# Kernel tuning notes

Hardware: AMD Instinct MI355X
Metric: run time of the kernel (lower is better)

## Reference

```python
import jax, jax.numpy as jnp
import numpy as np

C = 256      # bev_channels
K = 5        # deform kernel size
PAD = K // 2
T = K * K    # 25 taps
MID = C // 8 # channel-attn bottleneck
H, W = 100, 100
B = 1
GN_GROUPS = 8
EPS = 1e-5


def conv1x1(x, w, b=None):
    # x [B,Ci,H,W], w [Co,Ci]
    y = jnp.einsum('oc,bchw->bohw', w, x)
    if b is not None:
        y = y + b[None, :, None, None]
    return y


def conv3x3(x, w):
    # x [B,Ci,H,W], w [Co,Ci,3,3], stride 1, SAME padding
    return jax.lax.conv_general_dilated(
        x, w, (1, 1), 'SAME', dimension_numbers=('NCHW', 'OIHW', 'NCHW'))


def group_norm(x, gamma, beta, groups=GN_GROUPS, eps=EPS):
    b, c, h, w = x.shape
    xg = x.reshape(b, groups, c // groups, h, w)
    m = xg.mean((2, 3, 4), keepdims=True)
    v = xg.var((2, 3, 4), keepdims=True)
    xg = (xg - m) * jax.lax.rsqrt(v + eps)
    return xg.reshape(b, c, h, w) * gamma[None, :, None, None] + beta[None, :, None, None]


def deform_dw_conv(hist, offset, weight):
    """Depthwise deformable conv (torchvision semantics, deform_groups=1).
    hist [B,C,H,W], offset [B,2*T,H,W] as (dy,dx) pairs per tap (row-major taps),
    weight [C,1,K,K]. Zero-padding outside image (bilinear corners masked)."""
    b, c, h, w = hist.shape
    off = offset.reshape(b, T, 2, h, w)
    hg, wg = jnp.meshgrid(jnp.arange(h, dtype=hist.dtype),
                          jnp.arange(w, dtype=hist.dtype), indexing='ij')
    ky = (jnp.arange(T) // K - PAD).astype(hist.dtype)
    kx = (jnp.arange(T) % K - PAD).astype(hist.dtype)
    ys = hg[None, None] + ky[None, :, None, None] + off[:, :, 0]  # [B,T,H,W]
    xs = wg[None, None] + kx[None, :, None, None] + off[:, :, 1]

    def sample(img, yy, xx):  # img [C,H,W]; yy,xx [T,H,W]
        y0 = jnp.floor(yy)
        x0 = jnp.floor(xx)

        def gather(yc, xc):
            valid = (yc >= 0) & (yc <= h - 1) & (xc >= 0) & (xc <= w - 1)
            yi = jnp.clip(yc, 0, h - 1).astype(jnp.int32)
            xi = jnp.clip(xc, 0, w - 1).astype(jnp.int32)
            v = img.reshape(c, -1)[:, (yi * w + xi).reshape(-1)].reshape(c, T, h, w)
            return jnp.where(valid[None], v, jnp.zeros((), img.dtype))

        wy = yy - y0
        wx = xx - x0
        return (((1 - wy) * (1 - wx))[None] * gather(y0, x0)
                + ((1 - wy) * wx)[None] * gather(y0, x0 + 1)
                + (wy * (1 - wx))[None] * gather(y0 + 1, x0)
                + (wy * wx)[None] * gather(y0 + 1, x0 + 1))

    sampled = jax.vmap(sample)(hist, ys, xs)  # [B,C,T,H,W]
    return jnp.einsum('bcthw,ct->bchw', sampled, weight.reshape(c, T))


def ha_net(cur, hist, offset_w, offset_b, deform_w, ca_w1, ca_w2, out_w, gn_g, gn_b):
    offset = conv1x1(jnp.concatenate([cur, hist], axis=1), offset_w, offset_b)
    aligned = deform_dw_conv(hist, offset, deform_w)
    pooled = (cur - aligned).mean((2, 3))                    # AdaptiveAvgPool2d(1) -> [B,C]
    attn = jax.nn.sigmoid(jax.nn.relu(pooled @ ca_w1.T) @ ca_w2.T)[:, :, None, None]
    fused = cur + aligned * attn
    return jax.nn.relu(group_norm(conv3x3(fused, out_w), gn_g, gn_b))


def setup_inputs() -> dict:
    key = jax.random.key(0)
    ks = jax.random.split(key, 12)
    rn = lambda k, s, sc: jax.random.normal(k, s, jnp.float32) * sc
    return {
        'cur':   rn(ks[0], (B, C, H, W), 1.0),
        'hist0': rn(ks[1], (B, C, H, W), 1.0),
        'hist1': rn(ks[2], (B, C, H, W), 1.0),
        'offset_w': rn(ks[3], (2 * T, 2 * C), 0.01),
        'offset_b': jnp.zeros((2 * T,), jnp.float32),
        'deform_w': rn(ks[4], (C, 1, K, K), 0.2),
        'ca_w1': rn(ks[5], (MID, C), 0.05),
        'ca_w2': rn(ks[6], (C, MID), 0.05),
        'out_w': rn(ks[7], (C, C, 3, 3), 0.02),
        'gn_g': jnp.ones((C,), jnp.float32),
        'gn_b': jnp.zeros((C,), jnp.float32),
        'fuse_w': rn(ks[8], (C, C, 3, 3), 0.02),
        'bn_g': jnp.ones((C,), jnp.float32),
        'bn_b': jnp.zeros((C,), jnp.float32),
    }


def reference(cur, hist0, hist1, offset_w, offset_b, deform_w, ca_w1, ca_w2,
              out_w, gn_g, gn_b, fuse_w, bn_g, bn_b):
    aligned_sum = 0.0
    weight_sum = 0.0
    for hist in (hist0, hist1):  # fixed memory length = 2
        aligned = ha_net(cur, hist, offset_w, offset_b, deform_w,
                         ca_w1, ca_w2, out_w, gn_g, gn_b)
        diff = jnp.abs(cur - hist).mean((2, 3), keepdims=True)  # [B,C,1,1]
        wgt = jax.nn.sigmoid(-diff)
        aligned_sum = aligned_sum + aligned * wgt
        weight_sum = weight_sum + wgt
    fused = aligned_sum / (weight_sum + 1e-6)
    # fuse_conv: Conv3x3 -> BatchNorm2d (training: batch stats) -> ReLU
    y = conv3x3(fused, fuse_w)
    m = y.mean((0, 2, 3))
    v = y.var((0, 2, 3))
    y = (y - m[None, :, None, None]) * jax.lax.rsqrt(v + EPS)[None, :, None, None]
    y = y * bn_g[None, :, None, None] + bn_b[None, :, None, None]
    return jax.nn.relu(y)
```

## Files before the change

kernel.cpp:

```cpp
#include <hip/hip_runtime.h>
#include <hip/hip_bf16.h>

#define HW 10000
#define NC 256

typedef _Float16 h8 __attribute__((ext_vector_type(8)));
typedef float f32x4 __attribute__((ext_vector_type(4)));

#define RS 40

__device__ __forceinline__ int swz(int pos, int chunk) {
  return pos * RS + ((chunk ^ (pos & 3)) << 3);
}

#define WS_WMF     0
#define WS_ALIGNED 294912
#define WS_YBUF    2854912
#define WS_ASUM    5414912
#define WS_WOF     7974912
#define WS_POOLED  8007680
#define WS_ATTN    8007936
#define WS_WGT     8008192
#define WS_INVW    8008704
#define WS_GMV     8008960
#define WS_GNP     8008976

__device__ __forceinline__ float block_sum(float v, volatile float* sh) {
#pragma unroll
  for (int o = 32; o > 0; o >>= 1) v += __shfl_down(v, o);
  __syncthreads();
  if ((threadIdx.x & 63) == 0) sh[threadIdx.x >> 6] = v;
  __syncthreads();
  return sh[0] + sh[1] + sh[2] + sh[3];
}

__global__ void wprep_half(const float* __restrict__ W, int half, h8* __restrict__ Wmf) {
  const int id = blockIdx.x * 256 + threadIdx.x;
  const int lane = id & 63;
  int rest = id >> 6;
  const int s = rest & 1; rest >>= 1;
  const int tap = rest % 9; rest /= 9;
  const int c = rest & 7;
  const int cogl = rest >> 3;
  const int co = (half * 8 + cogl) * 16 + (lane & 15);
  const int ci0 = c * 32 + (lane >> 4) * 8;
  h8 frag;
#pragma unroll
  for (int j = 0; j < 8; j++) {
    const float w = W[(co * 256 + ci0 + j) * 9 + tap];
    const _Float16 hi = (_Float16)w;
    frag[j] = (s == 0) ? hi : (_Float16)((w - (float)hi) * 2048.f);
  }
  Wmf[id] = frag;
}

__global__ void wprep2(const float* __restrict__ W, h8* __restrict__ Wof) {
  const int id = blockIdx.x * 256 + threadIdx.x;
  const int lane = id & 63;
  int rest = id >> 6;
  const int g = rest & 3; rest >>= 2;
  const int s = rest & 1;
  const int c = rest >> 1;
  const int co = g * 16 + (lane & 15);
  const int ci0 = c * 32 + (lane >> 4) * 8;
  h8 frag;
#pragma unroll
  for (int j = 0; j < 8; j++) {
    const float w = (co < 50) ? W[co * 512 + ci0 + j] : 0.f;
    const _Float16 hi = (_Float16)w;
    frag[j] = (s == 0) ? hi : (_Float16)((w - (float)hi) * 2048.f);
  }
  Wof[id] = frag;
}

__global__ void gemm1x1_mfma(const float* __restrict__ cur, const float* __restrict__ hist,
                             const h8* __restrict__ Wof, const float* __restrict__ bias,
                             float* __restrict__ out) {
  __shared__ alignas(16) _Float16 Phi[64 * RS];
  __shared__ alignas(16) _Float16 Plo[64 * RS];
  const int t = threadIdx.x, lane = t & 63, wave = t >> 6;
  const int p0 = blockIdx.x * 64;
  const int nl = lane & 15, ksub = lane >> 4;
  f32x4 accM[4], accC[4], accL[4];
#pragma unroll
  for (int g = 0; g < 4; g++) { accM[g] = (f32x4)0.f; accC[g] = (f32x4)0.f; accL[g] = (f32x4)0.f; }
  const int bbase = swz(16 * wave + nl, ksub);

  for (int c = 0; c < 16; c++) {
    __syncthreads();
    for (int idx = t; idx < 1024; idx += 256) {
      const int cp = idx >> 6;
      const int pos = idx & 63;
      const int ci = c * 32 + cp * 2;
      const int p = p0 + pos;
      float v0 = 0.f, v1 = 0.f;
      if (p < HW) {
        v0 = (ci < NC) ? cur[ci * HW + p] : hist[(ci - NC) * HW + p];
        v1 = (ci + 1 < NC) ? cur[(ci + 1) * HW + p] : hist[(ci + 1 - NC) * HW + p];
      }
      const _Float16 h0 = (_Float16)v0, h1 = (_Float16)v1;
      const _Float16 l0 = (_Float16)((v0 - (float)h0) * 2048.f);
      const _Float16 l1 = (_Float16)((v1 - (float)h1) * 2048.f);
      const unsigned uh = (unsigned)__builtin_bit_cast(unsigned short, h0) |
                          ((unsigned)__builtin_bit_cast(unsigned short, h1) << 16);
      const unsigned ul = (unsigned)__builtin_bit_cast(unsigned short, l0) |
                          ((unsigned)__builtin_bit_cast(unsigned short, l1) << 16);
      const int ea = swz(pos, cp >> 2) + ((cp & 3) << 1);
      *(unsigned*)&Phi[ea] = uh;
      *(unsigned*)&Plo[ea] = ul;
    }
    __syncthreads();
    const h8 Bh = *(const h8*)&Phi[bbase];
    const h8 Bl = *(const h8*)&Plo[bbase];
#pragma unroll
    for (int g = 0; g < 4; g++) {
      const h8 Ah = Wof[((c * 2 + 0) * 4 + g) * 64 + lane];
      const h8 Al = Wof[((c * 2 + 1) * 4 + g) * 64 + lane];
      accM[g] = __builtin_amdgcn_mfma_f32_16x16x32_f16(Ah, Bh, accM[g], 0, 0, 0);
      accC[g] = __builtin_amdgcn_mfma_f32_16x16x32_f16(Ah, Bl, accC[g], 0, 0, 0);
      accC[g] = __builtin_amdgcn_mfma_f32_16x16x32_f16(Al, Bh, accC[g], 0, 0, 0);
      accL[g] = __builtin_amdgcn_mfma_f32_16x16x32_f16(Al, Bl, accL[g], 0, 0, 0);
    }
  }
#pragma unroll
  for (int g = 0; g < 4; g++) {
#pragma unroll
    for (int j = 0; j < 4; j++) {
      const int co = g * 16 + ksub * 4 + j;
      const int p = p0 + 16 * wave + nl;
      if (co < 50 && p < HW)
        out[co * HW + p] = accM[g][j] + accC[g][j] * (1.f / 2048.f) +
                           accL[g][j] * (1.f / 4194304.f) + bias[co];
    }
  }
}

__global__ void deform_kernel(const float* __restrict__ hist, const float* __restrict__ off,
                              const float* __restrict__ dw, float* __restrict__ aligned) {
  const int lane = threadIdx.x & 63;
  const int sub = threadIdx.x >> 6;
  const int p = blockIdx.x * 64 + lane;
  if (p >= HW) return;
  const int y = p / 100;
  const int x = p - y * 100;
  const int cbase = blockIdx.y * 32 + sub * 8;
  float acc[8];
#pragma unroll
  for (int k = 0; k < 8; k++) acc[k] = 0.f;

  for (int t = 0; t < 25; t++) {
    const float dy = off[(2 * t) * HW + p];
    const float dx = off[(2 * t + 1) * HW + p];
    const float ys = (float)(y + t / 5 - 2) + dy;
    const float xs = (float)(x + t % 5 - 2) + dx;
    const float y0f = floorf(ys), x0f = floorf(xs);
    const int y0 = (int)y0f, x0 = (int)x0f;
    const float wy = ys - y0f, wx = xs - x0f;
    const bool vy0 = (y0 >= 0) && (y0 <= 99);
    const bool vy1 = (y0 + 1 >= 0) && (y0 + 1 <= 99);
    const bool vx0 = (x0 >= 0) && (x0 <= 99);
    const bool vx1 = (x0 + 1 >= 0) && (x0 + 1 <= 99);
    const float w00 = (vy0 && vx0) ? (1.f - wy) * (1.f - wx) : 0.f;
    const float w01 = (vy0 && vx1) ? (1.f - wy) * wx : 0.f;
    const float w10 = (vy1 && vx0) ? wy * (1.f - wx) : 0.f;
    const float w11 = (vy1 && vx1) ? wy * wx : 0.f;
    const int yc0 = min(max(y0, 0), 99), yc1 = min(max(y0 + 1, 0), 99);
    const int xc0 = min(max(x0, 0), 99), xc1 = min(max(x0 + 1, 0), 99);
    const int i00 = yc0 * 100 + xc0, i01 = yc0 * 100 + xc1;
    const int i10 = yc1 * 100 + xc0, i11 = yc1 * 100 + xc1;
#pragma unroll
    for (int k = 0; k < 8; k++) {
      const float* hp = hist + (cbase + k) * HW;
      const float s = w00 * hp[i00] + w01 * hp[i01] + w10 * hp[i10] + w11 * hp[i11];
      acc[k] += dw[(cbase + k) * 25 + t] * s;
    }
  }
#pragma unroll
  for (int k = 0; k < 8; k++) aligned[(cbase + k) * HW + p] = acc[k];
}

__global__ void reduce_pw(const float* __restrict__ cur, const float* __restrict__ aligned,
                          const float* __restrict__ hist, float* __restrict__ pooled,
                          float* __restrict__ wgt) {
  __shared__ float sh[4];
  const int c = blockIdx.x;
  float s1 = 0.f, s2 = 0.f;
  for (int i = threadIdx.x; i < HW; i += 256) {
    const float cv = cur[c * HW + i];
    s1 += cv - aligned[c * HW + i];
    s2 += fabsf(cv - hist[c * HW + i]);
  }
  s1 = block_sum(s1, sh);
  s2 = block_sum(s2, sh);
  if (threadIdx.x == 0) {
    pooled[c] = s1 * (1.f / (float)HW);
    wgt[c] = 1.f / (1.f + expf(s2 * (1.f / (float)HW)));
  }
}

__global__ void attn_kernel(const float* __restrict__ pooled, const float* __restrict__ w1,
                            const float* __restrict__ w2, float* __restrict__ attn) {
  __shared__ float pl[256], hid[32];
  const int t = threadIdx.x;
  pl[t] = pooled[t];
  __syncthreads();
  if (t < 32) {
    float s = 0.f;
    for (int c = 0; c < 256; c++) s += w1[t * 256 + c] * pl[c];
    hid[t] = fmaxf(s, 0.f);
  }
  __syncthreads();
  float s = 0.f;
#pragma unroll
  for (int m = 0; m < 32; m++) s += w2[t * 32 + m] * hid[m];
  attn[t] = 1.f / (1.f + expf(-s));
}

__global__ void conv3x3_mfma(const float* __restrict__ X, const float* __restrict__ sx,
                             const float* __restrict__ Y, const h8* __restrict__ Wmf,
                             int half, float* __restrict__ out) {
  __shared__ alignas(16) _Float16 Phi[100 * RS];
  __shared__ alignas(16) _Float16 Plo[100 * RS];
  const int t = threadIdx.x, lane = t & 63, wave = t >> 6;
  const int ox0 = blockIdx.x * 8, oy0 = blockIdx.y * 8;
  const int wc = wave & 1, wn = wave >> 1;
  const int px0 = lane & 7, pyr = (lane >> 3) & 1, ksub = lane >> 4;

  f32x4 accM[4][2], accC[4][2], accL[4][2];
#pragma unroll
  for (int g = 0; g < 4; g++)
#pragma unroll
    for (int n = 0; n < 2; n++) {
      accM[g][n] = (f32x4)0.f; accC[g][n] = (f32x4)0.f; accL[g][n] = (f32x4)0.f;
    }

  int pbase[2];
#pragma unroll
  for (int n = 0; n < 2; n++)
    pbase[n] = (2 * (2 * wn + n) + pyr) * 10 + px0;

  for (int c = 0; c < 8; c++) {
    __syncthreads();
    for (int idx = t; idx < 1600; idx += 256) {
      const int cp = idx / 100;
      const int pos = idx - cp * 100;
      const int py = pos / 10, px = pos - py * 10;
      const int gy = oy0 - 1 + py, gx = ox0 - 1 + px;
      const int ci = c * 32 + cp * 2;
      float v0 = 0.f, v1 = 0.f;
      if (gy >= 0 && gy < 100 && gx >= 0 && gx < 100) {
        const int gi = gy * 100 + gx;
        v0 = X[ci * HW + gi] * sx[ci];
        v1 = X[(ci + 1) * HW + gi] * sx[ci + 1];
        if (Y) { v0 += Y[ci * HW + gi]; v1 += Y[(ci + 1) * HW + gi]; }
      }
      const _Float16 h0 = (_Float16)v0, h1 = (_Float16)v1;
      const _Float16 l0 = (_Float16)((v0 - (float)h0) * 2048.f);
      const _Float16 l1 = (_Float16)((v1 - (float)h1) * 2048.f);
      const unsigned uh = (unsigned)__builtin_bit_cast(unsigned short, h0) |
                          ((unsigned)__builtin_bit_cast(unsigned short, h1) << 16);
      const unsigned ul = (unsigned)__builtin_bit_cast(unsigned short, l0) |
                          ((unsigned)__builtin_bit_cast(unsigned short, l1) << 16);
      const int ea = swz(pos, cp >> 2) + ((cp & 3) << 1);
      *(unsigned*)&Phi[ea] = uh;
      *(unsigned*)&Plo[ea] = ul;
    }
    __syncthreads();
#pragma unroll
    for (int ky = 0; ky < 3; ky++) {
#pragma unroll
      for (int kx = 0; kx < 3; kx++) {
        const int tap = ky * 3 + kx;
        h8 Bh[2], Bl[2];
#pragma unroll
        for (int n = 0; n < 2; n++) {
          const int ba = swz(pbase[n] + ky * 10 + kx, ksub);
          Bh[n] = *(const h8*)&Phi[ba];
          Bl[n] = *(const h8*)&Plo[ba];
        }
#pragma unroll
        for (int g = 0; g < 4; g++) {
          const int cogl = wc * 4 + g;
          const h8* wp = Wmf + (size_t)(((cogl * 8 + c) * 9 + tap) * 2) * 64 + lane;
          const h8 Ah = wp[0];
          const h8 Al = wp[64];
#pragma unroll
          for (int n = 0; n < 2; n++) {
            accM[g][n] = __builtin_amdgcn_mfma_f32_16x16x32_f16(Ah, Bh[n], accM[g][n], 0, 0, 0);
            accC[g][n] = __builtin_amdgcn_mfma_f32_16x16x32_f16(Ah, Bl[n], accC[g][n], 0, 0, 0);
            accC[g][n] = __builtin_amdgcn_mfma_f32_16x16x32_f16(Al, Bh[n], accC[g][n], 0, 0, 0);
            accL[g][n] = __builtin_amdgcn_mfma_f32_16x16x32_f16(Al, Bl[n], accL[g][n], 0, 0, 0);
          }
        }
      }
    }
  }
#pragma unroll
  for (int g = 0; g < 4; g++) {
#pragma unroll
    for (int n = 0; n < 2; n++) {
      const int oy = oy0 + 2 * (2 * wn + n) + pyr;
      const int ox = ox0 + px0;
#pragma unroll
      for (int j = 0; j < 4; j++) {
        const int co = (half * 8 + wc * 4 + g) * 16 + ksub * 4 + j;
        if (oy < 100 && ox < 100)
          out[co * HW + oy * 100 + ox] = accM[g][n][j] + accC[g][n][j] * (1.f / 2048.f) +
                                         accL[g][n][j] * (1.f / 4194304.f);
      }
    }
  }
}

__global__ void gn_partial(const float* __restrict__ y, float* __restrict__ part) {
  __shared__ float sh[4];
  const int bx = blockIdx.x;
  const float* base = y + (size_t)bx * 4 * HW;
  float s = 0.f, ss = 0.f;
  for (int i = threadIdx.x; i < 4 * HW; i += 256) {
    const float v = base[i];
    s += v; ss += v * v;
  }
  s = block_sum(s, sh);
  ss = block_sum(ss, sh);
  if (threadIdx.x == 0) { part[bx] = s; part[64 + bx] = ss; }
}

__global__ void gn_final(const float* __restrict__ part, float* __restrict__ gmv) {
  const int g = threadIdx.x;
  if (g < 8) {
    float s = 0.f, ss = 0.f;
#pragma unroll
    for (int j = 0; j < 8; j++) { s += part[g * 8 + j]; ss += part[64 + g * 8 + j]; }
    const float m = s * (1.f / 320000.f);
    const float var = ss * (1.f / 320000.f) - m * m;
    gmv[g] = m;
    gmv[8 + g] = rsqrtf(var + 1e-5f);
  }
}

__global__ void gn_apply(const float* __restrict__ y, const float* __restrict__ gmv,
                         const float* __restrict__ gn_g, const float* __restrict__ gn_b,
                         const float* __restrict__ wgt, float* __restrict__ asum, int first) {
  const int c = blockIdx.x;
  const int g = c >> 5;
  const float m = gmv[g], rs = gmv[8 + g], ga = gn_g[c], be = gn_b[c], wg = wgt[c];
  for (int i = threadIdx.x; i < HW; i += 256) {
    const float v = fmaxf((y[c * HW + i] - m) * rs * ga + be, 0.f) * wg;
    if (first) asum[c * HW + i] = v;
    else asum[c * HW + i] += v;
  }
}

__global__ void invw_kernel(const float* __restrict__ wgt, float* __restrict__ invw) {
  const int c = threadIdx.x;
  invw[c] = 1.f / (wgt[c] + wgt[256 + c] + 1e-6f);
}

__global__ void bn_relu(const float* __restrict__ y, const float* __restrict__ bn_g,
                        const float* __restrict__ bn_b, float* __restrict__ out) {
  __shared__ float sh[4];
  const int c = blockIdx.x;
  float s = 0.f;
  for (int i = threadIdx.x; i < HW; i += 256) s += y[c * HW + i];
  const float m = block_sum(s, sh) * (1.f / (float)HW);
  float ss = 0.f;
  for (int i = threadIdx.x; i < HW; i += 256) {
    const float d = y[c * HW + i] - m;
    ss += d * d;
  }
  const float var = block_sum(ss, sh) * (1.f / (float)HW);
  const float rstd = rsqrtf(var + 1e-5f);
  const float ga = bn_g[c], be = bn_b[c];
  for (int i = threadIdx.x; i < HW; i += 256) {
    out[c * HW + i] = fmaxf((y[c * HW + i] - m) * rstd * ga + be, 0.f);
  }
}

extern "C" void kernel_launch(void* const* d_in, const int* in_sizes, int n_in,
                              void* d_out, int out_size, void* d_ws, size_t ws_size,
                              hipStream_t stream) {
  const float* cur      = (const float*)d_in[0];
  const float* hist0    = (const float*)d_in[1];
  const float* hist1    = (const float*)d_in[2];
  const float* offset_w = (const float*)d_in[3];
  const float* offset_b = (const float*)d_in[4];
  const float* deform_w = (const float*)d_in[5];
  const float* ca_w1    = (const float*)d_in[6];
  const float* ca_w2    = (const float*)d_in[7];
  const float* out_w    = (const float*)d_in[8];
  const float* gn_g     = (const float*)d_in[9];
  const float* gn_b     = (const float*)d_in[10];
  const float* fuse_w   = (const float*)d_in[11];
  const float* bn_g     = (const float*)d_in[12];
  const float* bn_b     = (const float*)d_in[13];

  float* ws       = (float*)d_ws;
  float* w_align  = ws + WS_ALIGNED;
  float* w_ybuf   = ws + WS_YBUF;
  float* w_off    = w_ybuf;
  float* w_asum   = ws + WS_ASUM;
  float* w_pooled = ws + WS_POOLED;
  float* w_attn   = ws + WS_ATTN;
  float* w_wgt    = ws + WS_WGT;
  float* w_invw   = ws + WS_INVW;
  float* w_gmv    = ws + WS_GMV;
  float* w_gnp    = ws + WS_GNP;
  h8* wmf = (h8*)(ws + WS_WMF);
  h8* wof = (h8*)(ws + WS_WOF);

  wprep2<<<32, 256, 0, stream>>>(offset_w, wof);

  const float* hists[2] = {hist0, hist1};
  for (int h = 0; h < 2; h++) {
    const float* hist = hists[h];
    gemm1x1_mfma<<<157, 256, 0, stream>>>(cur, hist, wof, offset_b, w_off);
    deform_kernel<<<dim3(157, 8), 256, 0, stream>>>(hist, w_off, deform_w, w_align);
    reduce_pw<<<256, 256, 0, stream>>>(cur, w_align, hist, w_pooled, w_wgt + h * 256);
    attn_kernel<<<1, 256, 0, stream>>>(w_pooled, ca_w1, ca_w2, w_attn);
    for (int half = 0; half < 2; half++) {
      wprep_half<<<288, 256, 0, stream>>>(out_w, half, wmf);
      conv3x3_mfma<<<dim3(13, 13), 256, 0, stream>>>(w_align, w_attn, cur, wmf, half, w_ybuf);
    }
    gn_partial<<<64, 256, 0, stream>>>(w_ybuf, w_gnp);
    gn_final<<<1, 64, 0, stream>>>(w_gnp, w_gmv);
    gn_apply<<<256, 256, 0, stream>>>(w_ybuf, w_gmv, gn_g, gn_b, w_wgt + h * 256, w_asum,
                                      h == 0 ? 1 : 0);
  }
  invw_kernel<<<1, 256, 0, stream>>>(w_wgt, w_invw);
  for (int half = 0; half < 2; half++) {
    wprep_half<<<288, 256, 0, stream>>>(fuse_w, half, wmf);
    conv3x3_mfma<<<dim3(13, 13), 256, 0, stream>>>(w_asum, w_invw, nullptr, wmf, half, w_ybuf);
  }
  bn_relu<<<256, 256, 0, stream>>>(w_ybuf, bn_g, bn_b, (float*)d_out);
}
```

Measured before the change: 1.837 ms.

## Enlarge conv3x3 spatial tile to 16x16 and stage weights in LDS

The 3x3 MFMA convolution now computes 16x16 output tiles instead of 8x8, with a z grid dimension splitting each half's output channels into two groups of 64. Weight fragments for each channel chunk are copied into shared memory and then read from there, and wprep_half writes them in a matching chunk-major layout. The goal is more input-halo reuse and fewer repeated global weight loads per MFMA. In exchange, each block uses much more LDS (about 126 KB) and more accumulator registers. The grid shrinks to 98 blocks, which may leave many CUs idle.

New measurement: 1.823 ms. No clear change (-0.8%).

```diff
diff --git a/kernel.cpp b/kernel.cpp
--- a/kernel.cpp
+++ b/kernel.cpp
@@ -37,12 +37,13 @@
 __global__ void wprep_half(const float* __restrict__ W, int half, h8* __restrict__ Wmf) {
   const int id = blockIdx.x * 256 + threadIdx.x;
   const int lane = id & 63;
-  int rest = id >> 6;
-  const int s = rest & 1; rest >>= 1;
-  const int tap = rest % 9; rest /= 9;
-  const int c = rest & 7;
-  const int cogl = rest >> 3;
-  const int co = (half * 8 + cogl) * 16 + (lane & 15);
+  int f = id >> 6;
+  const int s = f & 1; f >>= 1;
+  const int tap = f % 9; f /= 9;
+  const int cogl = f & 3; f >>= 2;
+  const int z = f & 1;
+  const int c = f >> 1;
+  const int co = ((half * 2 + z) * 4 + cogl) * 16 + (lane & 15);
   const int ci0 = c * 32 + (lane >> 4) * 8;
   h8 frag;
 #pragma unroll
@@ -51,7 +52,7 @@
     const _Float16 hi = (_Float16)w;
     frag[j] = (s == 0) ? hi : (_Float16)((w - (float)hi) * 2048.f);
   }
-  Wmf[id] = frag;
+  Wmf[(c * 2 + z) * 4608 + ((cogl * 9 + tap) * 2 + s) * 64 + lane] = frag;
 }
 
 __global__ void wprep2(const float* __restrict__ W, h8* __restrict__ Wof) {
@@ -216,35 +217,34 @@
   attn[t] = 1.f / (1.f + expf(-s));
 }
 
-__global__ void conv3x3_mfma(const float* __restrict__ X, const float* __restrict__ sx,
-                             const float* __restrict__ Y, const h8* __restrict__ Wmf,
-                             int half, float* __restrict__ out) {
-  __shared__ alignas(16) _Float16 Phi[100 * RS];
-  __shared__ alignas(16) _Float16 Plo[100 * RS];
+__launch_bounds__(256, 1)
+__global__ void conv3x3_v2(const float* __restrict__ X, const float* __restrict__ sx,
+                           const float* __restrict__ Y, const h8* __restrict__ Wmf,
+                           int half, float* __restrict__ out) {
+  __shared__ alignas(16) _Float16 Phi[324 * RS];
+  __shared__ alignas(16) _Float16 Plo[324 * RS];
+  __shared__ h8 Wl[4608];
   const int t = threadIdx.x, lane = t & 63, wave = t >> 6;
-  const int ox0 = blockIdx.x * 8, oy0 = blockIdx.y * 8;
-  const int wc = wave & 1, wn = wave >> 1;
-  const int px0 = lane & 7, pyr = (lane >> 3) & 1, ksub = lane >> 4;
-
-  f32x4 accM[4][2], accC[4][2], accL[4][2];
-#pragma unroll
-  for (int g = 0; g < 4; g++)
-#pragma unroll
-    for (int n = 0; n < 2; n++) {
-      accM[g][n] = (f32x4)0.f; accC[g][n] = (f32x4)0.f; accL[g][n] = (f32x4)0.f;
-    }
-
-  int pbase[2];
-#pragma unroll
-  for (int n = 0; n < 2; n++)
-    pbase[n] = (2 * (2 * wn + n) + pyr) * 10 + px0;
+  const int ox0 = blockIdx.x * 16, oy0 = blockIdx.y * 16;
+  const int z = blockIdx.z;
+  const int nl = lane & 15, ksub = lane >> 4;
+  const int cgbase = (wave & 1) * 2;
+  const int ngbase = (wave >> 1) * 8;
+
+  f32x4 aM[2][8], aC[2][8], aL[2][8];
+#pragma unroll
+  for (int cc = 0; cc < 2; cc++)
+#pragma unroll
+    for (int nn = 0; nn < 8; nn++) {
+      aM[cc][nn] = (f32x4)0.f; aC[cc][nn] = (f32x4)0.f; aL[cc][nn] = (f32x4)0.f;
+    }
 
   for (int c = 0; c < 8; c++) {
     __syncthreads();
-    for (int idx = t; idx < 1600; idx += 256) {
-      const int cp = idx / 100;
-      const int pos = idx - cp * 100;
-      const int py = pos / 10, px = pos - py * 10;
+    for (int idx = t; idx < 5184; idx += 256) {
+      const int cp = idx / 324;
+      const int pos = idx - cp * 324;
+      const int py = pos / 18, px = pos - py * 18;
       const int gy = oy0 - 1 + py, gx = ox0 - 1 + px;
       const int ci = c * 32 + cp * 2;
       float v0 = 0.f, v1 = 0.f;
@@ -265,48 +265,54 @@
       *(unsigned*)&Phi[ea] = uh;
       *(unsigned*)&Plo[ea] = ul;
     }
+    {
+      const h8* __restrict__ wg = Wmf + (c * 2 + z) * 4608;
+      for (int i = t; i < 4608; i += 256) Wl[i] = wg[i];
+    }
     __syncthreads();
 #pragma unroll
     for (int ky = 0; ky < 3; ky++) {
 #pragma unroll
       for (int kx = 0; kx < 3; kx++) {
         const int tap = ky * 3 + kx;
-        h8 Bh[2], Bl[2];
-#pragma unroll
-        for (int n = 0; n < 2; n++) {
-          const int ba = swz(pbase[n] + ky * 10 + kx, ksub);
-          Bh[n] = *(const h8*)&Phi[ba];
-          Bl[n] = *(const h8*)&Plo[ba];
+        h8 Ah[2], Al[2];
+#pragma unroll
+        for (int cc = 0; cc < 2; cc++) {
+          const int cogl = cgbase + cc;
+          Ah[cc] = Wl[((cogl * 9 + tap) * 2 + 0) * 64 + lane];
+          Al[cc] = Wl[((cogl * 9 + tap) * 2 + 1) * 64 + lane];
         }
 #pragma unroll
-        for (int g = 0; g < 4; g++) {
-          const int cogl = wc * 4 + g;
-          const h8* wp = Wmf + (size_t)(((cogl * 8 + c) * 9 + tap) * 2) * 64 + lane;
-          const h8 Ah = wp[0];
-          const h8 Al = wp[64];
-#pragma unroll
-          for (int n = 0; n < 2; n++) {
-            accM[g][n] = __builtin_amdgcn_mfma_f32_16x16x32_f16(Ah, Bh[n], accM[g][n], 0, 0, 0);
-            accC[g][n] = __builtin_amdgcn_mfma_f32_16x16x32_f16(Ah, Bl[n], accC[g][n], 0, 0, 0);
-            accC[g][n] = __builtin_amdgcn_mfma_f32_16x16x32_f16(Al, Bh[n], accC[g][n], 0, 0, 0);
-            accL[g][n] = __builtin_amdgcn_mfma_f32_16x16x32_f16(Al, Bl[n], accL[g][n], 0, 0, 0);
+        for (int nn = 0; nn < 8; nn++) {
+          const int row = (ngbase + nn + ky) * 18 + nl + kx;
+          const int ba = swz(row, ksub);
+          const h8 Bh = *(const h8*)&Phi[ba];
+          const h8 Bl = *(const h8*)&Plo[ba];
+#pragma unroll
+          for (int cc = 0; cc < 2; cc++) {
+            aM[cc][nn] = __builtin_amdgcn_mfma_f32_16x16x32_f16(Ah[cc], Bh, aM[cc][nn], 0, 0, 0);
+            aC[cc][nn] = __builtin_amdgcn_mfma_f32_16x16x32_f16(Ah[cc], Bl, aC[cc][nn], 0, 0, 0);
+            aC[cc][nn] = __builtin_amdgcn_mfma_f32_16x16x32_f16(Al[cc], Bh, aC[cc][nn], 0, 0, 0);
+            aL[cc][nn] = __builtin_amdgcn_mfma_f32_16x16x32_f16(Al[cc], Bl, aL[cc][nn], 0, 0, 0);
           }
         }
       }
     }
   }
-#pragma unroll
-  for (int g = 0; g < 4; g++) {
-#pragma unroll
-    for (int n = 0; n < 2; n++) {
-      const int oy = oy0 + 2 * (2 * wn + n) + pyr;
-      const int ox = ox0 + px0;
-#pragma unroll
-      for (int j = 0; j < 4; j++) {
-        const int co = (half * 8 + wc * 4 + g) * 16 + ksub * 4 + j;
-        if (oy < 100 && ox < 100)
-          out[co * HW + oy * 100 + ox] = accM[g][n][j] + accC[g][n][j] * (1.f / 2048.f) +
-                                         accL[g][n][j] * (1.f / 4194304.f);
+  const int ox = ox0 + nl;
+#pragma unroll
+  for (int cc = 0; cc < 2; cc++) {
+    const int co0 = ((half * 2 + z) * 4 + cgbase + cc) * 16 + ksub * 4;
+#pragma unroll
+    for (int nn = 0; nn < 8; nn++) {
+      const int oy = oy0 + ngbase + nn;
+      if (oy < 100 && ox < 100) {
+#pragma unroll
+        for (int j = 0; j < 4; j++) {
+          out[(co0 + j) * HW + oy * 100 + ox] =
+              aM[cc][nn][j] + aC[cc][nn][j] * (1.f / 2048.f) +
+              aL[cc][nn][j] * (1.f / 4194304.f);
+        }
       }
     }
   }
@@ -420,7 +426,7 @@
     attn_kernel<<<1, 256, 0, stream>>>(w_pooled, ca_w1, ca_w2, w_attn);
     for (int half = 0; half < 2; half++) {
       wprep_half<<<288, 256, 0, stream>>>(out_w, half, wmf);
-      conv3x3_mfma<<<dim3(13, 13), 256, 0, stream>>>(w_align, w_attn, cur, wmf, half, w_ybuf);
+      conv3x3_v2<<<dim3(7, 7, 2), 256, 0, stream>>>(w_align, w_attn, cur, wmf, half, w_ybuf);
     }
     gn_partial<<<64, 256, 0, stream>>>(w_ybuf, w_gnp);
     gn_final<<<1, 64, 0, stream>>>(w_gnp, w_gmv);
@@ -430,7 +436,7 @@
   invw_kernel<<<1, 256, 0, stream>>>(w_wgt, w_invw);
   for (int half = 0; half < 2; half++) {
     wprep_half<<<288, 256, 0, stream>>>(fuse_w, half, wmf);
-    conv3x3_mfma<<<dim3(13, 13), 256, 0, stream>>>(w_asum, w_invw, nullptr, wmf, half, w_ybuf);
+    conv3x3_v2<<<dim3(7, 7, 2), 256, 0, stream>>>(w_asum, w_invw, nullptr, wmf, half, w_ybuf);
   }
   bn_relu<<<256, 256, 0, stream>>>(w_ybuf, bn_g, bn_b, (float*)d_out);
 }
```
